# Performance work log

Measured on AMD Instinct MI355X. Metric: run time of the kernel, lower is better.

Reference implementation:

```python
import jax, jax.numpy as jnp
import numpy as np

DIM = 256
N_STATE = 8
DT_RANK = 16  # ceil(dim/16)
D_CONV = 4
HIDDEN = 128  # dim * rank_ratio
EPS = 1e-6


def rmsnorm(x, w):
    # matches torch: x / (||x||_2 / sqrt(d) + eps) * w
    norm = jnp.sqrt(jnp.sum(x * x, axis=-1, keepdims=True))
    return x / (norm / np.sqrt(x.shape[-1]) + EPS) * w


def dwconv1d(x, w, b, pad_l, pad_r):
    # x: (b, l, c); w: (c, 1, k) depthwise
    out = jax.lax.conv_general_dilated(
        x.transpose(0, 2, 1), w, window_strides=(1,),
        padding=[(pad_l, pad_r)], dimension_numbers=('NCH', 'OIH', 'NCH'),
        feature_group_count=w.shape[0])
    return (out + b[None, :, None]).transpose(0, 2, 1)


def selective_scan(x, delta, A, Bm, Cm, D):
    # x, delta: (b,l,d); A: (d,n); Bm, Cm: (b,l,n); D: (d,)
    dA = jnp.exp(delta[..., None] * A)                     # (b,l,d,n)
    dBx = (delta * x)[..., None] * Bm[:, :, None, :]       # (b,l,d,n)

    def step(h, inp):
        dA_t, dBx_t, C_t = inp
        h = dA_t * h + dBx_t                               # (b,d,n)
        y = jnp.einsum('bdn,bn->bd', h, C_t)
        return h, y

    h0 = jnp.zeros((x.shape[0],) + A.shape, dtype=x.dtype)
    _, ys = jax.lax.scan(step, h0,
                         (dA.transpose(1, 0, 2, 3), dBx.transpose(1, 0, 2, 3),
                          Cm.transpose(1, 0, 2)))
    return ys.transpose(1, 0, 2) + x * D                   # (b,l,d)


def mamba_branch(x, ctx, conv_w, conv_b, xproj_w, dtproj_w, dtproj_b, A_log, D):
    xc = jax.nn.silu(dwconv1d(x, conv_w, conv_b, D_CONV - 1, 0))  # causal conv
    x_dbl = ctx @ xproj_w.T                                  # (b,l,r+2n)
    dt, Bm, Cm = jnp.split(x_dbl, [DT_RANK, DT_RANK + N_STATE], axis=-1)
    delta = jax.nn.softplus(dt @ dtproj_w.T + dtproj_b)
    A = -jnp.exp(A_log)
    return selective_scan(xc, delta, A, Bm, Cm, D)


def setup_inputs() -> dict:
    key = jax.random.key(0)
    ks = jax.random.split(key, 24)
    B, L, D = 4, 64 * 64, DIM
    s = 0.02
    A_log_init = jnp.log(jnp.broadcast_to(jnp.arange(1, N_STATE + 1, dtype=jnp.float32), (D, N_STATE)))
    dt_bias = jnp.full((D,), jnp.log(jnp.expm1(0.01)), dtype=jnp.float32)
    inp = {
        'x0': jax.random.normal(ks[0], (B, L, D), jnp.float32),
        'x1': jax.random.normal(ks[1], (B, L, D), jnp.float32),
        'w_norm0': jnp.ones((D,), jnp.float32),
        'w_norm1': jnp.ones((D,), jnp.float32),
        'in_proj_w': jax.random.normal(ks[2], (2 * D, D), jnp.float32) * s,
        'conv_w_f': jax.random.normal(ks[3], (D, 1, D_CONV), jnp.float32) * 0.3,
        'conv_b_f': jnp.zeros((D,), jnp.float32),
        'xproj_w_f': jax.random.normal(ks[4], (DT_RANK + 2 * N_STATE, D), jnp.float32) * s,
        'dtproj_w_f': jax.random.normal(ks[5], (D, DT_RANK), jnp.float32) * 0.1,
        'dtproj_b_f': dt_bias,
        'A_log_f': A_log_init,
        'D_f': jnp.ones((D,), jnp.float32),
        'conv_w_bw': jax.random.normal(ks[6], (D, 1, D_CONV), jnp.float32) * 0.3,
        'conv_b_bw': jnp.zeros((D,), jnp.float32),
        'xproj_w_bw': jax.random.normal(ks[7], (DT_RANK + 2 * N_STATE, D), jnp.float32) * s,
        'dtproj_w_bw': jax.random.normal(ks[8], (D, DT_RANK), jnp.float32) * 0.1,
        'dtproj_b_bw': dt_bias,
        'A_log_bw': A_log_init,
        'D_bw': jnp.ones((D,), jnp.float32),
        'norm_y_w': jnp.ones((D,), jnp.float32),
        'out_proj_w': jax.random.normal(ks[9], (D, D), jnp.float32) * s,
        'fc1_w': jax.random.normal(ks[10], (HIDDEN, D), jnp.float32) * s,
        'dw_w': jax.random.normal(ks[11], (HIDDEN, 1, 3), jnp.float32) * 0.3,
        'dw_b': jnp.zeros((HIDDEN,), jnp.float32),
        'fc2_w': jax.random.normal(ks[12], (D, HIDDEN), jnp.float32) * s,
    }
    return inp


def reference(x0, x1, w_norm0, w_norm1, in_proj_w, conv_w_f, conv_b_f, xproj_w_f,
              dtproj_w_f, dtproj_b_f, A_log_f, D_f, conv_w_bw, conv_b_bw,
              xproj_w_bw, dtproj_w_bw, dtproj_b_bw, A_log_bw, D_bw, norm_y_w,
              out_proj_w, fc1_w, dw_w, dw_b, fc2_w):
    residual = x0
    h0 = rmsnorm(x0, w_norm0)
    h1 = rmsnorm(x1, w_norm1)
    # cross-Mamba: main stream x0 -> x,z; extra_emb x1 -> dt/B/C
    xz = h0 @ in_proj_w.T
    xin, z = jnp.split(xz, 2, axis=-1)
    y_f = mamba_branch(xin, h1, conv_w_f, conv_b_f, xproj_w_f, dtproj_w_f,
                       dtproj_b_f, A_log_f, D_f)
    y_b = jnp.flip(mamba_branch(jnp.flip(xin, 1), jnp.flip(h1, 1), conv_w_bw,
                                conv_b_bw, xproj_w_bw, dtproj_w_bw, dtproj_b_bw,
                                A_log_bw, D_bw), 1)
    y = (y_f + y_b) * 0.5          # if_devide_out=True (bidirectional)
    y = rmsnorm(y, norm_y_w)       # use_norm=True
    y = y * jax.nn.silu(z)
    x = y @ out_proj_w.T + residual
    # LowRankFeedForward (dropout = identity at eval)
    m = x @ fc1_w.T
    m = jax.nn.silu(dwconv1d(m, dw_w, dw_b, 1, 1))
    m = m @ fc2_w.T
    return x + m
```

## Files before the change

### kernel.cpp

```cpp
#include <hip/hip_runtime.h>
#include <math.h>
#include <cstddef>

#define BB 4
#define LL 4096
#define DD 256
#define NST 8
#define RANK 16
#define HID 128
#define BL (BB*LL)
#define BLD ((size_t)BL*DD)
#define CH 256
#define CLEN 16
#define XZS 512

typedef __bf16 bf16x8 __attribute__((ext_vector_type(8)));
typedef float  f32x4  __attribute__((ext_vector_type(4)));

__device__ __forceinline__ float siluf(float x){ return x / (1.f + __expf(-x)); }
__device__ __forceinline__ float softplus_fast(float x){
  float r = __logf(1.f + __expf(x));
  return x > 15.f ? x : r;
}
__device__ __forceinline__ unsigned short f2bf(float x){
  union { float f; unsigned u; } v; v.f = x;
  unsigned r = v.u + 0x7fffu + ((v.u >> 16) & 1u);
  return (unsigned short)(r >> 16);
}
__device__ __forceinline__ float bf2f(unsigned short u){
  union { unsigned u32; float f; } c; c.u32 = ((unsigned)u) << 16;
  return c.f;
}

__global__ __launch_bounds__(256) void pre_kernel(
    const float* __restrict__ x0, const float* __restrict__ w0, unsigned short* __restrict__ o0b,
    const float* __restrict__ x1, const float* __restrict__ w1, unsigned short* __restrict__ o1b,
    const float* __restrict__ sA,
    const float* __restrict__ s0, const float* __restrict__ s1,
    const float* __restrict__ s2, const float* __restrict__ s3,
    const float* __restrict__ s4,
    unsigned short* __restrict__ d1, unsigned short* __restrict__ d2)
{
  int blk = blockIdx.x;
  if (blk < 8192){
    const float* x; const float* w; unsigned short* o; size_t tok;
    int wv = threadIdx.x >> 6, lane = threadIdx.x & 63;
    if (blk < 4096){ x = x0; w = w0; o = o0b; tok = (size_t)blk*4 + wv; }
    else           { x = x1; w = w1; o = o1b; tok = (size_t)(blk-4096)*4 + wv; }
    float4 v = ((const float4*)(x + tok*DD))[lane];
    float s = v.x*v.x + v.y*v.y + v.z*v.z + v.w*v.w;
    #pragma unroll
    for (int m = 1; m < 64; m <<= 1) s += __shfl_xor(s, m, 64);
    float scale = 1.f / (sqrtf(s) * (1.f/16.f) + 1e-6f);
    float4 wvv = ((const float4*)w)[lane];
    ushort4 r;
    r.x = f2bf(v.x*scale*wvv.x); r.y = f2bf(v.y*scale*wvv.y);
    r.z = f2bf(v.z*scale*wvv.z); r.w = f2bf(v.w*scale*wvv.w);
    ((ushort4*)(o + tok*DD))[lane] = r;
    return;
  }
  int i = (blk - 8192)*256 + threadIdx.x;
  if (i >= 278528) return;
  if (i < 131072){ d1[i] = f2bf(sA[i]); return; }
  int j = i - 131072;
  float v;
  if (j < 8192)        v = s0[j];
  else if (j < 16384)  v = s1[j - 8192];
  else if (j < 81920)  v = s2[j - 16384];
  else if (j < 114688) v = s3[j - 81920];
  else                 v = s4[j - 114688];
  d2[j] = f2bf(v);
}

template<int EPI>
__global__ __launch_bounds__(256) void gemm_mfma(
    const unsigned short* __restrict__ A, const unsigned short* __restrict__ Bw,
    float* __restrict__ C, const float* __restrict__ Add,
    unsigned short* __restrict__ Cb, int M, int ldc, int K)
{
  constexpr int BK = 64, PAD = 8;
  __shared__ __align__(16) unsigned short As[64][BK+PAD];
  __shared__ __align__(16) unsigned short Bs[64][BK+PAD];
  int tid  = threadIdx.x;
  int row0 = blockIdx.x * 64;
  int col0 = blockIdx.y * 64;
  int wave = tid >> 6, lane = tid & 63;
  int wm = (wave >> 1) * 32, wn = (wave & 1) * 32;
  int lm = lane & 15, kq = lane >> 4;
  int sr = tid >> 2, sc16 = (tid & 3) * 16;

  f32x4 acc[2][2];
  #pragma unroll
  for (int i = 0; i < 2; i++)
    #pragma unroll
    for (int j = 0; j < 2; j++) acc[i][j] = (f32x4){0.f,0.f,0.f,0.f};

  for (int k0 = 0; k0 < K; k0 += BK){
    const unsigned short* ap = &A [(size_t)(row0 + sr)*K + k0 + sc16];
    const unsigned short* bp = &Bw[(size_t)(col0 + sr)*K + k0 + sc16];
    *(int4*)&As[sr][sc16]   = *(const int4*)ap;
    *(int4*)&As[sr][sc16+8] = *(const int4*)(ap + 8);
    *(int4*)&Bs[sr][sc16]   = *(const int4*)bp;
    *(int4*)&Bs[sr][sc16+8] = *(const int4*)(bp + 8);
    __syncthreads();
    #pragma unroll
    for (int ks = 0; ks < 2; ks++){
      bf16x8 af[2], bfv[2];
      #pragma unroll
      for (int i = 0; i < 2; i++) af[i]  = *(const bf16x8*)&As[wm + i*16 + lm][ks*32 + kq*8];
      #pragma unroll
      for (int j = 0; j < 2; j++) bfv[j] = *(const bf16x8*)&Bs[wn + j*16 + lm][ks*32 + kq*8];
      #pragma unroll
      for (int i = 0; i < 2; i++)
        #pragma unroll
        for (int j = 0; j < 2; j++)
          acc[i][j] = __builtin_amdgcn_mfma_f32_16x16x32_bf16(af[i], bfv[j], acc[i][j], 0, 0, 0);
    }
    __syncthreads();
  }

  #pragma unroll
  for (int i = 0; i < 2; i++){
    int rbase = row0 + wm + i*16 + kq*4;
    #pragma unroll
    for (int j = 0; j < 2; j++){
      int col = col0 + wn + j*16 + lm;
      #pragma unroll
      for (int r = 0; r < 4; r++){
        size_t idx = (size_t)(rbase + r)*ldc + col;
        float v = acc[i][j][r];
        if constexpr (EPI == 2) v += Add[idx];
        if constexpr (EPI != 3) C[idx] = v;
        if constexpr (EPI == 3) Cb[idx] = f2bf(v);
      }
    }
  }
}

__global__ __launch_bounds__(256) void gemm_xzxp(
    const unsigned short* __restrict__ A0, const unsigned short* __restrict__ A1,
    const unsigned short* __restrict__ B0, const unsigned short* __restrict__ B1,
    unsigned short* __restrict__ Cxz, float* __restrict__ Cxd)
{
  constexpr int BK = 64, PAD = 8, K = 256;
  __shared__ __align__(16) unsigned short As[64][BK+PAD];
  __shared__ __align__(16) unsigned short Bs[64][BK+PAD];
  int tid  = threadIdx.x;
  bool xp  = (blockIdx.y == 8);
  const unsigned short* A  = xp ? A1 : A0;
  const unsigned short* Bw = xp ? B1 : B0;
  int row0 = blockIdx.x * 64;
  int col0 = xp ? 0 : blockIdx.y * 64;
  int wave = tid >> 6, lane = tid & 63;
  int wm = (wave >> 1) * 32, wn = (wave & 1) * 32;
  int lm = lane & 15, kq = lane >> 4;
  int sr = tid >> 2, sc16 = (tid & 3) * 16;

  f32x4 acc[2][2];
  #pragma unroll
  for (int i = 0; i < 2; i++)
    #pragma unroll
    for (int j = 0; j < 2; j++) acc[i][j] = (f32x4){0.f,0.f,0.f,0.f};

  for (int k0 = 0; k0 < K; k0 += BK){
    const unsigned short* ap = &A [(size_t)(row0 + sr)*K + k0 + sc16];
    const unsigned short* bp = &Bw[(size_t)(col0 + sr)*K + k0 + sc16];
    *(int4*)&As[sr][sc16]   = *(const int4*)ap;
    *(int4*)&As[sr][sc16+8] = *(const int4*)(ap + 8);
    *(int4*)&Bs[sr][sc16]   = *(const int4*)bp;
    *(int4*)&Bs[sr][sc16+8] = *(const int4*)(bp + 8);
    __syncthreads();
    #pragma unroll
    for (int ks = 0; ks < 2; ks++){
      bf16x8 af[2], bfv[2];
      #pragma unroll
      for (int i = 0; i < 2; i++) af[i]  = *(const bf16x8*)&As[wm + i*16 + lm][ks*32 + kq*8];
      #pragma unroll
      for (int j = 0; j < 2; j++) bfv[j] = *(const bf16x8*)&Bs[wn + j*16 + lm][ks*32 + kq*8];
      #pragma unroll
      for (int i = 0; i < 2; i++)
        #pragma unroll
        for (int j = 0; j < 2; j++)
          acc[i][j] = __builtin_amdgcn_mfma_f32_16x16x32_bf16(af[i], bfv[j], acc[i][j], 0, 0, 0);
    }
    __syncthreads();
  }

  #pragma unroll
  for (int i = 0; i < 2; i++){
    int rbase = row0 + wm + i*16 + kq*4;
    #pragma unroll
    for (int j = 0; j < 2; j++){
      int col = col0 + wn + j*16 + lm;
      #pragma unroll
      for (int r = 0; r < 4; r++){
        float v = acc[i][j][r];
        if (xp) Cxd[(size_t)(rbase + r)*64  + col] = v;
        else    Cxz[(size_t)(rbase + r)*XZS + col] = f2bf(v);
      }
    }
  }
}

__global__ __launch_bounds__(256) void gemm_fc1(
    const float* __restrict__ A, const unsigned short* __restrict__ Bw,
    float* __restrict__ C)
{
  constexpr int BK = 64, PAD = 8, K = 256, LDC = 128;
  __shared__ __align__(16) unsigned short As[64][BK+PAD];
  __shared__ __align__(16) unsigned short Bs[64][BK+PAD];
  int tid  = threadIdx.x;
  int row0 = blockIdx.x * 64;
  int col0 = blockIdx.y * 64;
  int wave = tid >> 6, lane = tid & 63;
  int wm = (wave >> 1) * 32, wn = (wave & 1) * 32;
  int lm = lane & 15, kq = lane >> 4;
  int sr = tid >> 2, sc16 = (tid & 3) * 16;

  f32x4 acc[2][2];
  #pragma unroll
  for (int i = 0; i < 2; i++)
    #pragma unroll
    for (int j = 0; j < 2; j++) acc[i][j] = (f32x4){0.f,0.f,0.f,0.f};

  for (int k0 = 0; k0 < K; k0 += BK){
    const float* ap = &A[(size_t)(row0 + sr)*K + k0 + sc16];
    #pragma unroll
    for (int q = 0; q < 4; q++){
      float4 f = *(const float4*)(ap + q*4);
      ushort4 u; u.x = f2bf(f.x); u.y = f2bf(f.y); u.z = f2bf(f.z); u.w = f2bf(f.w);
      *(ushort4*)&As[sr][sc16 + q*4] = u;
    }
    const unsigned short* bp = &Bw[(size_t)(col0 + sr)*K + k0 + sc16];
    *(int4*)&Bs[sr][sc16]   = *(const int4*)bp;
    *(int4*)&Bs[sr][sc16+8] = *(const int4*)(bp + 8);
    __syncthreads();
    #pragma unroll
    for (int ks = 0; ks < 2; ks++){
      bf16x8 af[2], bfv[2];
      #pragma unroll
      for (int i = 0; i < 2; i++) af[i]  = *(const bf16x8*)&As[wm + i*16 + lm][ks*32 + kq*8];
      #pragma unroll
      for (int j = 0; j < 2; j++) bfv[j] = *(const bf16x8*)&Bs[wn + j*16 + lm][ks*32 + kq*8];
      #pragma unroll
      for (int i = 0; i < 2; i++)
        #pragma unroll
        for (int j = 0; j < 2; j++)
          acc[i][j] = __builtin_amdgcn_mfma_f32_16x16x32_bf16(af[i], bfv[j], acc[i][j], 0, 0, 0);
    }
    __syncthreads();
  }

  #pragma unroll
  for (int i = 0; i < 2; i++){
    int rbase = row0 + wm + i*16 + kq*4;
    #pragma unroll
    for (int j = 0; j < 2; j++){
      int col = col0 + wn + j*16 + lm;
      #pragma unroll
      for (int r = 0; r < 4; r++)
        C[(size_t)(rbase + r)*LDC + col] = acc[i][j][r];
    }
  }
}

__global__ __launch_bounds__(256) void gemm_fc2dw(
    const float* __restrict__ m1, const unsigned short* __restrict__ Bw,
    const float* __restrict__ dww, const float* __restrict__ dwb,
    float* __restrict__ C)
{
  constexpr int BK = 64, PAD = 8, K = 128, LDC = 256;
  __shared__ __align__(16) unsigned short As[64][BK+PAD];
  __shared__ __align__(16) unsigned short Bs[64][BK+PAD];
  __shared__ float wS[HID*3];
  __shared__ float bS[HID];
  int tid  = threadIdx.x;
  if (tid < HID){
    bS[tid] = dwb[tid];
    wS[tid*3+0] = dww[tid*3+0];
    wS[tid*3+1] = dww[tid*3+1];
    wS[tid*3+2] = dww[tid*3+2];
  }
  __syncthreads();

  int row0 = blockIdx.x * 64;
  int col0 = blockIdx.y * 64;
  int wave = tid >> 6, lane = tid & 63;
  int wm = (wave >> 1) * 32, wn = (wave & 1) * 32;
  int lm = lane & 15, kq = lane >> 4;
  int sr = tid >> 2, sc16 = (tid & 3) * 16;
  int r16 = tid >> 4, cc = (tid & 15) * 4;

  f32x4 acc[2][2];
  #pragma unroll
  for (int i = 0; i < 2; i++)
    #pragma unroll
    for (int j = 0; j < 2; j++) acc[i][j] = (f32x4){0.f,0.f,0.f,0.f};

  for (int k0 = 0; k0 < K; k0 += BK){
    #pragma unroll
    for (int pp = 0; pp < 4; pp++){
      int r = pp*16 + r16;
      int t = row0 + r;
      int tl = t & (LL-1);
      int c = k0 + cc;
      const float* mrow = &m1[(size_t)t*HID + c];
      float4 vm = *(const float4*)mrow;
      float4 vp = (tl > 0)      ? *(const float4*)(mrow - HID) : (float4){0,0,0,0};
      float4 vn = (tl < LL-1)   ? *(const float4*)(mrow + HID) : (float4){0,0,0,0};
      float a0 = bS[c+0] + wS[(c+0)*3]*vp.x + wS[(c+0)*3+1]*vm.x + wS[(c+0)*3+2]*vn.x;
      float a1 = bS[c+1] + wS[(c+1)*3]*vp.y + wS[(c+1)*3+1]*vm.y + wS[(c+1)*3+2]*vn.y;
      float a2 = bS[c+2] + wS[(c+2)*3]*vp.z + wS[(c+2)*3+1]*vm.z + wS[(c+2)*3+2]*vn.z;
      float a3 = bS[c+3] + wS[(c+3)*3]*vp.w + wS[(c+3)*3+1]*vm.w + wS[(c+3)*3+2]*vn.w;
      ushort4 u;
      u.x = f2bf(siluf(a0)); u.y = f2bf(siluf(a1));
      u.z = f2bf(siluf(a2)); u.w = f2bf(siluf(a3));
      *(ushort4*)&As[r][cc] = u;
    }
    const unsigned short* bp = &Bw[(size_t)(col0 + sr)*K + k0 + sc16];
    *(int4*)&Bs[sr][sc16]   = *(const int4*)bp;
    *(int4*)&Bs[sr][sc16+8] = *(const int4*)(bp + 8);
    __syncthreads();
    #pragma unroll
    for (int ks = 0; ks < 2; ks++){
      bf16x8 af[2], bfv[2];
      #pragma unroll
      for (int i = 0; i < 2; i++) af[i]  = *(const bf16x8*)&As[wm + i*16 + lm][ks*32 + kq*8];
      #pragma unroll
      for (int j = 0; j < 2; j++) bfv[j] = *(const bf16x8*)&Bs[wn + j*16 + lm][ks*32 + kq*8];
      #pragma unroll
      for (int i = 0; i < 2; i++)
        #pragma unroll
        for (int j = 0; j < 2; j++)
          acc[i][j] = __builtin_amdgcn_mfma_f32_16x16x32_bf16(af[i], bfv[j], acc[i][j], 0, 0, 0);
    }
    __syncthreads();
  }

  #pragma unroll
  for (int i = 0; i < 2; i++){
    int rbase = row0 + wm + i*16 + kq*4;
    #pragma unroll
    for (int j = 0; j < 2; j++){
      int col = col0 + wn + j*16 + lm;
      #pragma unroll
      for (int r = 0; r < 4; r++){
        size_t idx = (size_t)(rbase + r)*LDC + col;
        C[idx] = C[idx] + acc[i][j][r];
      }
    }
  }
}

__global__ __launch_bounds__(256) void front_kernel(
    const unsigned short* __restrict__ xz,
    const float* __restrict__ xd,
    const float* __restrict__ cwf, const float* __restrict__ cbf,
    const float* __restrict__ cwb, const float* __restrict__ cbb,
    const float* __restrict__ dtwf, const float* __restrict__ dtbf,
    const float* __restrict__ dtwb, const float* __restrict__ dtbb,
    const float* __restrict__ Alogf, const float* __restrict__ Alogb,
    const float* __restrict__ Dfp, const float* __restrict__ Dbp,
    unsigned int* __restrict__ xde,
    float* __restrict__ Sp, float* __restrict__ Hout)
{
  int chunk = blockIdx.x, b = blockIdx.y, dir = blockIdx.z;
  int s0 = chunk*CLEN;
  int d  = threadIdx.x;

  __shared__ float sdt[CLEN][16];
  __shared__ float sB [CLEN][8];
  __shared__ float sC [CLEN][8];
  #pragma unroll
  for (int e = threadIdx.x; e < CLEN*32; e += 256){
    int lt = e >> 5, col = e & 31;
    int pos = s0 + lt;
    int row = dir ? (LL-1-pos) : pos;
    float v = xd[((size_t)b*LL + row)*64 + dir*32 + col];
    if (col < 16)      sdt[lt][col]    = v;
    else if (col < 24) sB [lt][col-16] = v;
    else               sC [lt][col-24] = v;
  }
  __syncthreads();

  float4 cw = ((const float4*)(dir ? cwb : cwf))[d];
  float cb  = (dir ? cbb : cbf)[d];
  const float* dtw = (dir ? dtwb : dtwf) + d*RANK;
  float4 w0 = ((const float4*)dtw)[0], w1 = ((const float4*)dtw)[1];
  float4 w2 = ((const float4*)dtw)[2], w3 = ((const float4*)dtw)[3];
  float dtb = (dir ? dtbb : dtbf)[d];
  float Dd  = (dir ? Dbp : Dfp)[d];

  const unsigned short* xp = xz + (size_t)b*LL*XZS + d;
  #define LDX(pos) ((pos) >= 0 ? bf2f(xp[(size_t)(dir ? (LL-1-(pos)) : (pos))*XZS]) : 0.f)

  float xv[CLEN+3];
  xv[0] = LDX(s0-3); xv[1] = LDX(s0-2); xv[2] = LDX(s0-1);
  #pragma unroll
  for (int i = 0; i < CLEN; i++) xv[3+i] = LDX(s0+i);
  #undef LDX

  unsigned packX[CLEN];
  #pragma unroll
  for (int i = 0; i < CLEN; i++){
    float xc = cb;
    xc = fmaf(cw.x, xv[i],   xc); xc = fmaf(cw.y, xv[i+1], xc);
    xc = fmaf(cw.z, xv[i+2], xc); xc = fmaf(cw.w, xv[i+3], xc);
    xc = siluf(xc);
    const float* dt = &sdt[i][0];
    float de = dtb;
    de = fmaf(dt[0],w0.x, fmaf(dt[1],w0.y, fmaf(dt[2],w0.z, fmaf(dt[3],w0.w, de))));
    de = fmaf(dt[4],w1.x, fmaf(dt[5],w1.y, fmaf(dt[6],w1.z, fmaf(dt[7],w1.w, de))));
    de = fmaf(dt[8],w2.x, fmaf(dt[9],w2.y, fmaf(dt[10],w2.z, fmaf(dt[11],w2.w, de))));
    de = fmaf(dt[12],w3.x, fmaf(dt[13],w3.y, fmaf(dt[14],w3.z, fmaf(dt[15],w3.w, de))));
    de = softplus_fast(de);
    packX[i] = (unsigned)f2bf(xc) | ((unsigned)f2bf(de) << 16);
  }

  const float* Alog = dir ? Alogb : Alogf;
  float A[NST];
  bool fast = true;
  #pragma unroll
  for (int n = 0; n < NST; n++){
    A[n] = -__expf(Alog[d*NST + n]);
    fast = fast && (fabsf(A[n] + (float)(n+1)) < 1e-3f);
  }
  float h[NST];
  #pragma unroll
  for (int n = 0; n < NST; n++) h[n] = 0.f;
  float S = 0.f;

  unsigned int* xout = xde + ((size_t)(dir*BB + b)*LL + s0)*DD + d;

  if (fast){
    #pragma unroll
    for (int t = 0; t < CLEN; t++){
      unsigned pk = packX[t];
      float xc = bf2f((unsigned short)(pk & 0xffffu));
      float de = bf2f((unsigned short)(pk >> 16));
      S += de;
      float dux = de * xc;
      const float* Bv = &sB[t][0];
      const float* Cv = &sC[t][0];
      float e1 = __expf(-de);
      float dA = e1;
      float acc = xc * Dd;
      h[0] = fmaf(dA, h[0], dux*Bv[0]); acc = fmaf(h[0], Cv[0], acc); dA *= e1;
      h[1] = fmaf(dA, h[1], dux*Bv[1]); acc = fmaf(h[1], Cv[1], acc); dA *= e1;
      h[2] = fmaf(dA, h[2], dux*Bv[2]); acc = fmaf(h[2], Cv[2], acc); dA *= e1;
      h[3] = fmaf(dA, h[3], dux*Bv[3]); acc = fmaf(h[3], Cv[3], acc); dA *= e1;
      h[4] = fmaf(dA, h[4], dux*Bv[4]); acc = fmaf(h[4], Cv[4], acc); dA *= e1;
      h[5] = fmaf(dA, h[5], dux*Bv[5]); acc = fmaf(h[5], Cv[5], acc); dA *= e1;
      h[6] = fmaf(dA, h[6], dux*Bv[6]); acc = fmaf(h[6], Cv[6], acc); dA *= e1;
      h[7] = fmaf(dA, h[7], dux*Bv[7]); acc = fmaf(h[7], Cv[7], acc);
      xout[(size_t)t*DD] = (pk & 0xffff0000u) | (unsigned)f2bf(acc);
    }
  } else {
    #pragma unroll
    for (int t = 0; t < CLEN; t++){
      unsigned pk = packX[t];
      float xc = bf2f((unsigned short)(pk & 0xffffu));
      float de = bf2f((unsigned short)(pk >> 16));
      S += de;
      float dux = de * xc;
      const float* Bv = &sB[t][0];
      const float* Cv = &sC[t][0];
      float acc = xc * Dd;
      #pragma unroll
      for (int n = 0; n < NST; n++){
        h[n] = fmaf(__expf(de*A[n]), h[n], dux*Bv[n]);
        acc = fmaf(h[n], Cv[n], acc);
      }
      xout[(size_t)t*DD] = (pk & 0xffff0000u) | (unsigned)f2bf(acc);
    }
  }

  size_t ob = ((((size_t)dir*CH + chunk)*BB + b)*DD + d)*NST;
  float4 h0v, h1v;
  h0v.x=h[0]; h0v.y=h[1]; h0v.z=h[2]; h0v.w=h[3];
  h1v.x=h[4]; h1v.y=h[5]; h1v.z=h[6]; h1v.w=h[7];
  *(float4*)&Hout[ob]   = h0v; *(float4*)&Hout[ob+4] = h1v;
  Sp[((size_t)(dir*CH + chunk)*BB + b)*DD + d] = S;
}

__global__ __launch_bounds__(64) void scan_p2(
    const float* __restrict__ Sp, float* H,
    const float* __restrict__ Alogf, const float* __restrict__ Alogb)
{
  const int SEGC = CH/8;
  int blk = blockIdx.x;
  int d   = blk & (DD-1);
  int b   = (blk >> 8) & (BB-1);
  int dir = blk >> 10;
  int t   = threadIdx.x;
  int seg = t >> 3, n = t & 7;
  float A = -__expf((dir ? Alogb : Alogf)[d*NST + n]);

  const size_t sstr = (size_t)BB*DD;
  const size_t hstr = (size_t)BB*DD*NST;
  size_t sb = (size_t)dir*CH*sstr + (size_t)b*DD + d;
  size_t hb = (size_t)dir*CH*hstr + ((size_t)b*DD + d)*NST + n;
  int c0 = seg*SEGC;

  float pv[SEGC], hv[SEGC];
  #pragma unroll
  for (int k = 0; k < SEGC; k++){
    pv[k] = Sp[sb + (size_t)(c0+k)*sstr];
    hv[k] = H [hb + (size_t)(c0+k)*hstr];
  }
  float h = 0.f, Ss = 0.f;
  #pragma unroll
  for (int k = 0; k < SEGC; k++){
    Ss += pv[k];
    pv[k] = __expf(pv[k]*A);
    h = fmaf(pv[k], h, hv[k]);
  }
  float pi = __expf(Ss*A), hi = h;
  #pragma unroll
  for (int off = 8; off < 64; off <<= 1){
    float hprev = __shfl_up(hi, off, 64);
    float pprev = __shfl_up(pi, off, 64);
    if (t >= off){ hi = fmaf(pi, hprev, hi); pi *= pprev; }
  }
  float hin = __shfl_up(hi, 8, 64);
  h = (seg == 0) ? 0.f : hin;
  #pragma unroll
  for (int k = 0; k < SEGC; k++){
    size_t idx = hb + (size_t)(c0+k)*hstr;
    H[idx] = h;
    h = fmaf(pv[k], h, hv[k]);
  }
}

__global__ __launch_bounds__(256) void back_kernel(
    const unsigned int* __restrict__ xde,
    const float* __restrict__ xd,
    const float* __restrict__ Alogf, const float* __restrict__ Alogb,
    const float* __restrict__ Hin,
    const unsigned short* __restrict__ xz,
    const float* __restrict__ wn,
    unsigned short* __restrict__ outb)
{
  int c  = blockIdx.x, b = blockIdx.y;
  int cbk = CH-1-c;
  int d  = threadIdx.x;
  int T0 = c*CLEN;
  int Pb = cbk*CLEN;

  __shared__ float sCf[CLEN][8], sCb[CLEN][8];
  __shared__ float red[CLEN][4];
  __shared__ float sscale[CLEN];
  {
    int k  = threadIdx.x & 7;
    int lt = (threadIdx.x >> 3) & 15;
    if (threadIdx.x < 128)
      sCf[lt][k] = xd[((size_t)b*LL + T0 + lt)*64 + 24 + k];
    else
      sCb[lt][k] = xd[((size_t)b*LL + (T0 + 15 - lt))*64 + 56 + k];
  }
  __syncthreads();

  float Af[NST], Ab[NST];
  bool fast = true;
  #pragma unroll
  for (int n = 0; n < NST; n++){
    Af[n] = -__expf(Alogf[d*NST + n]);
    Ab[n] = -__expf(Alogb[d*NST + n]);
    fast = fast && (fabsf(Af[n] + (float)(n+1)) < 1e-3f)
                && (fabsf(Ab[n] + (float)(n+1)) < 1e-3f);
  }

  float vf[CLEN];

  {
    float hn[NST];
    size_t ib = (((size_t)c*BB + b)*DD + d)*NST;
    float4 a0 = *(const float4*)&Hin[ib];
    float4 a1 = *(const float4*)&Hin[ib+4];
    hn[0]=a0.x; hn[1]=a0.y; hn[2]=a0.z; hn[3]=a0.w;
    hn[4]=a1.x; hn[5]=a1.y; hn[6]=a1.z; hn[7]=a1.w;
    const unsigned int* p = xde + ((size_t)b*LL + T0)*DD + d;
    unsigned int pk[CLEN];
    #pragma unroll
    for (int t = 0; t < CLEN; t++) pk[t] = p[(size_t)t*DD];
    float S = 0.f;
    if (fast){
      #pragma unroll
      for (int t = 0; t < CLEN; t++){
        float y0 = bf2f((unsigned short)(pk[t] & 0xffffu));
        float de = bf2f((unsigned short)(pk[t] >> 16));
        S += de;
        float E = __expf(-S);
        float q = E;
        float corr = q * (hn[0]*sCf[t][0]);
        q *= E; corr = fmaf(q, hn[1]*sCf[t][1], corr);
        q *= E; corr = fmaf(q, hn[2]*sCf[t][2], corr);
        q *= E; corr = fmaf(q, hn[3]*sCf[t][3], corr);
        q *= E; corr = fmaf(q, hn[4]*sCf[t][4], corr);
        q *= E; corr = fmaf(q, hn[5]*sCf[t][5], corr);
        q *= E; corr = fmaf(q, hn[6]*sCf[t][6], corr);
        q *= E; corr = fmaf(q, hn[7]*sCf[t][7], corr);
        vf[t] = y0 + corr;
      }
    } else {
      #pragma unroll
      for (int t = 0; t < CLEN; t++){
        float y0 = bf2f((unsigned short)(pk[t] & 0xffffu));
        float de = bf2f((unsigned short)(pk[t] >> 16));
        S += de;
        float corr = 0.f;
        #pragma unroll
        for (int n = 0; n < NST; n++)
          corr = fmaf(__expf(S*Af[n]), hn[n]*sCf[t][n], corr);
        vf[t] = y0 + corr;
      }
    }
  }

  {
    float hn[NST];
    size_t ib = ((((size_t)CH + cbk)*BB + b)*DD + d)*NST;
    float4 a0 = *(const float4*)&Hin[ib];
    float4 a1 = *(const float4*)&Hin[ib+4];
    hn[0]=a0.x; hn[1]=a0.y; hn[2]=a0.z; hn[3]=a0.w;
    hn[4]=a1.x; hn[5]=a1.y; hn[6]=a1.z; hn[7]=a1.w;
    const unsigned int* p = xde + ((size_t)(BB + b)*LL + Pb)*DD + d;
    unsigned int pk[CLEN];
    #pragma unroll
    for (int t = 0; t < CLEN; t++) pk[t] = p[(size_t)t*DD];
    float S = 0.f;
    if (fast){
      #pragma unroll
      for (int t = 0; t < CLEN; t++){
        float y0 = bf2f((unsigned short)(pk[t] & 0xffffu));
        float de = bf2f((unsigned short)(pk[t] >> 16));
        S += de;
        float E = __expf(-S);
        float q = E;
        float corr = q * (hn[0]*sCb[t][0]);
        q *= E; corr = fmaf(q, hn[1]*sCb[t][1], corr);
        q *= E; corr = fmaf(q, hn[2]*sCb[t][2], corr);
        q *= E; corr = fmaf(q, hn[3]*sCb[t][3], corr);
        q *= E; corr = fmaf(q, hn[4]*sCb[t][4], corr);
        q *= E; corr = fmaf(q, hn[5]*sCb[t][5], corr);
        q *= E; corr = fmaf(q, hn[6]*sCb[t][6], corr);
        q *= E; corr = fmaf(q, hn[7]*sCb[t][7], corr);
        int j = 15 - t;
        vf[j] = 0.5f*(vf[j] + y0 + corr);
      }
    } else {
      #pragma unroll
      for (int t = 0; t < CLEN; t++){
        float y0 = bf2f((unsigned short)(pk[t] & 0xffffu));
        float de = bf2f((unsigned short)(pk[t] >> 16));
        S += de;
        float corr = 0.f;
        #pragma unroll
        for (int n = 0; n < NST; n++)
          corr = fmaf(__expf(S*Ab[n]), hn[n]*sCb[t][n], corr);
        int j = 15 - t;
        vf[j] = 0.5f*(vf[j] + y0 + corr);
      }
    }
  }

  int wave = d >> 6, lane = d & 63;
  #pragma unroll
  for (int j = 0; j < CLEN; j++){
    float s = vf[j]*vf[j];
    #pragma unroll
    for (int m = 1; m < 64; m <<= 1) s += __shfl_xor(s, m, 64);
    if (lane == 0) red[j][wave] = s;
  }
  __syncthreads();
  if (d < CLEN){
    float s = red[d][0] + red[d][1] + red[d][2] + red[d][3];
    sscale[d] = 1.f / (sqrtf(s)*(1.f/16.f) + 1e-6f);
  }
  __syncthreads();

  float wd = wn[d];
  #pragma unroll
  for (int j = 0; j < CLEN; j++){
    size_t tok = (size_t)b*LL + T0 + j;
    float z = bf2f(xz[tok*XZS + 256 + d]);
    outb[tok*DD + d] = f2bf(vf[j]*sscale[j]*wd*siluf(z));
  }
}

extern "C" void kernel_launch(void* const* d_in, const int* in_sizes, int n_in,
                              void* d_out, int out_size, void* d_ws, size_t ws_size,
                              hipStream_t stream)
{
  const float* x0        = (const float*)d_in[0];
  const float* x1        = (const float*)d_in[1];
  const float* w_norm0   = (const float*)d_in[2];
  const float* w_norm1   = (const float*)d_in[3];
  const float* in_proj_w = (const float*)d_in[4];
  const float* conv_w_f  = (const float*)d_in[5];
  const float* conv_b_f  = (const float*)d_in[6];
  const float* xproj_w_f = (const float*)d_in[7];
  const float* dtproj_w_f= (const float*)d_in[8];
  const float* dtproj_b_f= (const float*)d_in[9];
  const float* A_log_f   = (const float*)d_in[10];
  const float* D_f       = (const float*)d_in[11];
  const float* conv_w_bw = (const float*)d_in[12];
  const float* conv_b_bw = (const float*)d_in[13];
  const float* xproj_w_bw= (const float*)d_in[14];
  const float* dtproj_w_bw=(const float*)d_in[15];
  const float* dtproj_b_bw=(const float*)d_in[16];
  const float* A_log_bw  = (const float*)d_in[17];
  const float* D_bw      = (const float*)d_in[18];
  const float* norm_y_w  = (const float*)d_in[19];
  const float* out_proj_w= (const float*)d_in[20];
  const float* fc1_w     = (const float*)d_in[21];
  const float* dw_w      = (const float*)d_in[22];
  const float* dw_b      = (const float*)d_in[23];
  const float* fc2_w     = (const float*)d_in[24];
  float* out = (float*)d_out;
  float* ws  = (float*)d_ws;

  float* r0 = ws + 0*BLD;
  float* r1 = ws + 1*BLD;
  float* r2 = ws + 2*BLD;
  float* r3 = ws + 3*BLD;
  float* r4 = ws + 4*BLD;
  float* r5 = ws + 5*BLD;
  float* r6 = ws + 6*BLD;
  float* r7 = ws + 7*BLD;

  unsigned short* h0b   = (unsigned short*)r0;
  unsigned short* h1b   = (unsigned short*)r1;
  unsigned short* xz_b  = (unsigned short*)r2;
  float*          xd    = r3;
  unsigned int*   xde   = (unsigned int*)r4;
  unsigned short* wbuf1 = (unsigned short*)r6;
  float* Hout = r6;
  float* Hin  = Hout;
  const size_t SPLANE = (size_t)2*CH*BB*DD;
  float* Sp   = r7 + (BLD - SPLANE);
  unsigned short* ycomb_b = (unsigned short*)r0;
  unsigned short* wbuf2   = (unsigned short*)r7;
  unsigned short* wb_xp   = wbuf2;
  unsigned short* wb_out  = wbuf2 + 16384;
  unsigned short* wb_fc1  = wbuf2 + 81920;
  unsigned short* wb_fc2  = wbuf2 + 114688;
  float*          m1      = r4;

  pre_kernel<<<dim3(9280), 256, 0, stream>>>(
      x0, w_norm0, h0b, x1, w_norm1, h1b,
      in_proj_w, xproj_w_f, xproj_w_bw, out_proj_w, fc1_w, fc2_w, wbuf1, wbuf2);

  gemm_xzxp<<<dim3(BL/64, 9), 256, 0, stream>>>(
      h0b, h1b, wbuf1, wb_xp, xz_b, xd);

  front_kernel<<<dim3(CH, BB, 2), 256, 0, stream>>>(
      xz_b, xd, conv_w_f, conv_b_f, conv_w_bw, conv_b_bw,
      dtproj_w_f, dtproj_b_f, dtproj_w_bw, dtproj_b_bw,
      A_log_f, A_log_bw, D_f, D_bw, xde, Sp, Hout);

  scan_p2<<<dim3(2*BB*DD), 64, 0, stream>>>(Sp, Hout, A_log_f, A_log_bw);

  back_kernel<<<dim3(CH, BB), 256, 0, stream>>>(
      xde, xd, A_log_f, A_log_bw, Hin, xz_b, norm_y_w, ycomb_b);

  gemm_mfma<2><<<dim3(BL/64, 4), 256, 0, stream>>>(
      ycomb_b, wb_out, out, x0, nullptr, BL, 256, 256);

  gemm_fc1<<<dim3(BL/64, 2), 256, 0, stream>>>(out, wb_fc1, m1);

  gemm_fc2dw<<<dim3(BL/64, 4), 256, 0, stream>>>(m1, wb_fc2, dw_w, dw_b, out);
}
```

Measured before the change: 251.8 us.

## Load full-K GEMM tiles via global_load_lds into XOR-swizzled LDS

All four GEMM kernels now stage the entire K extent of the A and B tiles into LDS once, replacing the K-loop of 64-wide chunks with one barrier each. Bf16 operands are copied straight from global memory to LDS with the global_load_lds builtin, and the padded layout is replaced by an XOR swizzle to avoid bank conflicts. This removes per-chunk synchronisation and the trip through registers. In exchange LDS use per block rises to about 64KB, which may reduce occupancy, and there is no overlap between loading and MFMA work inside a block.

```diff
diff --git a/kernel.cpp b/kernel.cpp
--- a/kernel.cpp
+++ b/kernel.cpp
@@ -32,6 +32,15 @@
   return c.f;
 }
 
+#define GLD16(gp, lp) __builtin_amdgcn_global_load_lds( \
+    (const __attribute__((address_space(1))) unsigned int*)(gp), \
+    (__attribute__((address_space(3))) unsigned int*)(lp), 16, 0, 0)
+
+#define LDSGK(base, row, g, GPR) \
+  (*(const bf16x8*)((base) + ((((row)*(GPR)) + ((g) ^ ((row)&7))) << 3)))
+#define LDSW4(base, row, col, GPR, u) \
+  *(ushort4*)((base) + ((((row)*(GPR)) + ((((col)>>3)) ^ ((row)&7))) << 3) + ((col)&7)) = (u)
+
 __global__ __launch_bounds__(256) void pre_kernel(
     const float* __restrict__ x0, const float* __restrict__ w0, unsigned short* __restrict__ o0b,
     const float* __restrict__ x1, const float* __restrict__ w1, unsigned short* __restrict__ o1b,
@@ -72,15 +81,140 @@
   d2[j] = f2bf(v);
 }
 
-template<int EPI>
+template<int EPI, int K>
 __global__ __launch_bounds__(256) void gemm_mfma(
     const unsigned short* __restrict__ A, const unsigned short* __restrict__ Bw,
-    float* __restrict__ C, const float* __restrict__ Add,
-    unsigned short* __restrict__ Cb, int M, int ldc, int K)
-{
-  constexpr int BK = 64, PAD = 8;
-  __shared__ __align__(16) unsigned short As[64][BK+PAD];
-  __shared__ __align__(16) unsigned short Bs[64][BK+PAD];
+    float* __restrict__ C, const float* __restrict__ Add, int ldc)
+{
+  constexpr int GPR = K/8;
+  constexpr int NI  = GPR/4;
+  __shared__ __align__(16) unsigned short AsL[64*K];
+  __shared__ __align__(16) unsigned short BsL[64*K];
+  int tid  = threadIdx.x;
+  int row0 = blockIdx.x * 64;
+  int col0 = blockIdx.y * 64;
+  int wave = tid >> 6, lane = tid & 63;
+  int wm = (wave >> 1) * 32, wn = (wave & 1) * 32;
+  int lm = lane & 15, kq = lane >> 4;
+
+  #pragma unroll
+  for (int i = 0; i < NI; i++){
+    int q  = (wave*NI + i)*64 + lane;
+    int r  = q / GPR, gq = q % GPR;
+    int g  = gq ^ (r & 7);
+    GLD16(A  + (size_t)(row0 + r)*K + g*8, AsL + (wave*NI + i)*512);
+    GLD16(Bw + (size_t)(col0 + r)*K + g*8, BsL + (wave*NI + i)*512);
+  }
+  __syncthreads();
+
+  f32x4 acc[2][2];
+  #pragma unroll
+  for (int i = 0; i < 2; i++)
+    #pragma unroll
+    for (int j = 0; j < 2; j++) acc[i][j] = (f32x4){0.f,0.f,0.f,0.f};
+
+  #pragma unroll
+  for (int ks = 0; ks < K/32; ks++){
+    bf16x8 af[2], bfv[2];
+    #pragma unroll
+    for (int i = 0; i < 2; i++) af[i]  = LDSGK(AsL, wm + i*16 + lm, ks*4 + kq, GPR);
+    #pragma unroll
+    for (int j = 0; j < 2; j++) bfv[j] = LDSGK(BsL, wn + j*16 + lm, ks*4 + kq, GPR);
+    #pragma unroll
+    for (int i = 0; i < 2; i++)
+      #pragma unroll
+      for (int j = 0; j < 2; j++)
+        acc[i][j] = __builtin_amdgcn_mfma_f32_16x16x32_bf16(af[i], bfv[j], acc[i][j], 0, 0, 0);
+  }
+
+  #pragma unroll
+  for (int i = 0; i < 2; i++){
+    int rbase = row0 + wm + i*16 + kq*4;
+    #pragma unroll
+    for (int j = 0; j < 2; j++){
+      int col = col0 + wn + j*16 + lm;
+      #pragma unroll
+      for (int r = 0; r < 4; r++){
+        size_t idx = (size_t)(rbase + r)*ldc + col;
+        float v = acc[i][j][r];
+        if constexpr (EPI == 2) v += Add[idx];
+        C[idx] = v;
+      }
+    }
+  }
+}
+
+__global__ __launch_bounds__(256) void gemm_xzxp(
+    const unsigned short* __restrict__ A0i, const unsigned short* __restrict__ A1i,
+    const unsigned short* __restrict__ B0i, const unsigned short* __restrict__ B1i,
+    unsigned short* __restrict__ Cxz, float* __restrict__ Cxd)
+{
+  constexpr int K = 256, GPR = K/8, NI = GPR/4;
+  __shared__ __align__(16) unsigned short AsL[64*K];
+  __shared__ __align__(16) unsigned short BsL[64*K];
+  int tid  = threadIdx.x;
+  bool xp  = (blockIdx.y == 8);
+  const unsigned short* A  = xp ? A1i : A0i;
+  const unsigned short* Bw = xp ? B1i : B0i;
+  int row0 = blockIdx.x * 64;
+  int col0 = xp ? 0 : blockIdx.y * 64;
+  int wave = tid >> 6, lane = tid & 63;
+  int wm = (wave >> 1) * 32, wn = (wave & 1) * 32;
+  int lm = lane & 15, kq = lane >> 4;
+
+  #pragma unroll
+  for (int i = 0; i < NI; i++){
+    int q  = (wave*NI + i)*64 + lane;
+    int r  = q / GPR, gq = q % GPR;
+    int g  = gq ^ (r & 7);
+    GLD16(A  + (size_t)(row0 + r)*K + g*8, AsL + (wave*NI + i)*512);
+    GLD16(Bw + (size_t)(col0 + r)*K + g*8, BsL + (wave*NI + i)*512);
+  }
+  __syncthreads();
+
+  f32x4 acc[2][2];
+  #pragma unroll
+  for (int i = 0; i < 2; i++)
+    #pragma unroll
+    for (int j = 0; j < 2; j++) acc[i][j] = (f32x4){0.f,0.f,0.f,0.f};
+
+  #pragma unroll
+  for (int ks = 0; ks < K/32; ks++){
+    bf16x8 af[2], bfv[2];
+    #pragma unroll
+    for (int i = 0; i < 2; i++) af[i]  = LDSGK(AsL, wm + i*16 + lm, ks*4 + kq, GPR);
+    #pragma unroll
+    for (int j = 0; j < 2; j++) bfv[j] = LDSGK(BsL, wn + j*16 + lm, ks*4 + kq, GPR);
+    #pragma unroll
+    for (int i = 0; i < 2; i++)
+      #pragma unroll
+      for (int j = 0; j < 2; j++)
+        acc[i][j] = __builtin_amdgcn_mfma_f32_16x16x32_bf16(af[i], bfv[j], acc[i][j], 0, 0, 0);
+  }
+
+  #pragma unroll
+  for (int i = 0; i < 2; i++){
+    int rbase = row0 + wm + i*16 + kq*4;
+    #pragma unroll
+    for (int j = 0; j < 2; j++){
+      int col = col0 + wn + j*16 + lm;
+      #pragma unroll
+      for (int r = 0; r < 4; r++){
+        float v = acc[i][j][r];
+        if (xp) Cxd[(size_t)(rbase + r)*64  + col] = v;
+        else    Cxz[(size_t)(rbase + r)*XZS + col] = f2bf(v);
+      }
+    }
+  }
+}
+
+__global__ __launch_bounds__(256) void gemm_fc1(
+    const float* __restrict__ Afp, const unsigned short* __restrict__ Bw,
+    float* __restrict__ C)
+{
+  constexpr int K = 256, GPR = K/8, NI = GPR/4, LDC = 128;
+  __shared__ __align__(16) unsigned short AsL[64*K];
+  __shared__ __align__(16) unsigned short BsL[64*K];
   int tid  = threadIdx.x;
   int row0 = blockIdx.x * 64;
   int col0 = blockIdx.y * 64;
@@ -89,166 +223,43 @@
   int lm = lane & 15, kq = lane >> 4;
   int sr = tid >> 2, sc16 = (tid & 3) * 16;
 
-  f32x4 acc[2][2];
-  #pragma unroll
-  for (int i = 0; i < 2; i++)
-    #pragma unroll
-    for (int j = 0; j < 2; j++) acc[i][j] = (f32x4){0.f,0.f,0.f,0.f};
-
-  for (int k0 = 0; k0 < K; k0 += BK){
-    const unsigned short* ap = &A [(size_t)(row0 + sr)*K + k0 + sc16];
-    const unsigned short* bp = &Bw[(size_t)(col0 + sr)*K + k0 + sc16];
-    *(int4*)&As[sr][sc16]   = *(const int4*)ap;
-    *(int4*)&As[sr][sc16+8] = *(const int4*)(ap + 8);
-    *(int4*)&Bs[sr][sc16]   = *(const int4*)bp;
-    *(int4*)&Bs[sr][sc16+8] = *(const int4*)(bp + 8);
-    __syncthreads();
-    #pragma unroll
-    for (int ks = 0; ks < 2; ks++){
-      bf16x8 af[2], bfv[2];
-      #pragma unroll
-      for (int i = 0; i < 2; i++) af[i]  = *(const bf16x8*)&As[wm + i*16 + lm][ks*32 + kq*8];
-      #pragma unroll
-      for (int j = 0; j < 2; j++) bfv[j] = *(const bf16x8*)&Bs[wn + j*16 + lm][ks*32 + kq*8];
-      #pragma unroll
-      for (int i = 0; i < 2; i++)
-        #pragma unroll
-        for (int j = 0; j < 2; j++)
-          acc[i][j] = __builtin_amdgcn_mfma_f32_16x16x32_bf16(af[i], bfv[j], acc[i][j], 0, 0, 0);
-    }
-    __syncthreads();
-  }
-
-  #pragma unroll
-  for (int i = 0; i < 2; i++){
-    int rbase = row0 + wm + i*16 + kq*4;
-    #pragma unroll
-    for (int j = 0; j < 2; j++){
-      int col = col0 + wn + j*16 + lm;
-      #pragma unroll
-      for (int r = 0; r < 4; r++){
-        size_t idx = (size_t)(rbase + r)*ldc + col;
-        float v = acc[i][j][r];
-        if constexpr (EPI == 2) v += Add[idx];
-        if constexpr (EPI != 3) C[idx] = v;
-        if constexpr (EPI == 3) Cb[idx] = f2bf(v);
-      }
-    }
-  }
-}
-
-__global__ __launch_bounds__(256) void gemm_xzxp(
-    const unsigned short* __restrict__ A0, const unsigned short* __restrict__ A1,
-    const unsigned short* __restrict__ B0, const unsigned short* __restrict__ B1,
-    unsigned short* __restrict__ Cxz, float* __restrict__ Cxd)
-{
-  constexpr int BK = 64, PAD = 8, K = 256;
-  __shared__ __align__(16) unsigned short As[64][BK+PAD];
-  __shared__ __align__(16) unsigned short Bs[64][BK+PAD];
-  int tid  = threadIdx.x;
-  bool xp  = (blockIdx.y == 8);
-  const unsigned short* A  = xp ? A1 : A0;
-  const unsigned short* Bw = xp ? B1 : B0;
-  int row0 = blockIdx.x * 64;
-  int col0 = xp ? 0 : blockIdx.y * 64;
-  int wave = tid >> 6, lane = tid & 63;
-  int wm = (wave >> 1) * 32, wn = (wave & 1) * 32;
-  int lm = lane & 15, kq = lane >> 4;
-  int sr = tid >> 2, sc16 = (tid & 3) * 16;
-
-  f32x4 acc[2][2];
-  #pragma unroll
-  for (int i = 0; i < 2; i++)
-    #pragma unroll
-    for (int j = 0; j < 2; j++) acc[i][j] = (f32x4){0.f,0.f,0.f,0.f};
-
-  for (int k0 = 0; k0 < K; k0 += BK){
-    const unsigned short* ap = &A [(size_t)(row0 + sr)*K + k0 + sc16];
-    const unsigned short* bp = &Bw[(size_t)(col0 + sr)*K + k0 + sc16];
-    *(int4*)&As[sr][sc16]   = *(const int4*)ap;
-    *(int4*)&As[sr][sc16+8] = *(const int4*)(ap + 8);
-    *(int4*)&Bs[sr][sc16]   = *(const int4*)bp;
-    *(int4*)&Bs[sr][sc16+8] = *(const int4*)(bp + 8);
-    __syncthreads();
-    #pragma unroll
-    for (int ks = 0; ks < 2; ks++){
-      bf16x8 af[2], bfv[2];
-      #pragma unroll
-      for (int i = 0; i < 2; i++) af[i]  = *(const bf16x8*)&As[wm + i*16 + lm][ks*32 + kq*8];
-      #pragma unroll
-      for (int j = 0; j < 2; j++) bfv[j] = *(const bf16x8*)&Bs[wn + j*16 + lm][ks*32 + kq*8];
-      #pragma unroll
-      for (int i = 0; i < 2; i++)
-        #pragma unroll
-        for (int j = 0; j < 2; j++)
-          acc[i][j] = __builtin_amdgcn_mfma_f32_16x16x32_bf16(af[i], bfv[j], acc[i][j], 0, 0, 0);
-    }
-    __syncthreads();
-  }
-
-  #pragma unroll
-  for (int i = 0; i < 2; i++){
-    int rbase = row0 + wm + i*16 + kq*4;
-    #pragma unroll
-    for (int j = 0; j < 2; j++){
-      int col = col0 + wn + j*16 + lm;
-      #pragma unroll
-      for (int r = 0; r < 4; r++){
-        float v = acc[i][j][r];
-        if (xp) Cxd[(size_t)(rbase + r)*64  + col] = v;
-        else    Cxz[(size_t)(rbase + r)*XZS + col] = f2bf(v);
-      }
-    }
-  }
-}
-
-__global__ __launch_bounds__(256) void gemm_fc1(
-    const float* __restrict__ A, const unsigned short* __restrict__ Bw,
-    float* __restrict__ C)
-{
-  constexpr int BK = 64, PAD = 8, K = 256, LDC = 128;
-  __shared__ __align__(16) unsigned short As[64][BK+PAD];
-  __shared__ __align__(16) unsigned short Bs[64][BK+PAD];
-  int tid  = threadIdx.x;
-  int row0 = blockIdx.x * 64;
-  int col0 = blockIdx.y * 64;
-  int wave = tid >> 6, lane = tid & 63;
-  int wm = (wave >> 1) * 32, wn = (wave & 1) * 32;
-  int lm = lane & 15, kq = lane >> 4;
-  int sr = tid >> 2, sc16 = (tid & 3) * 16;
-
-  f32x4 acc[2][2];
-  #pragma unroll
-  for (int i = 0; i < 2; i++)
-    #pragma unroll
-    for (int j = 0; j < 2; j++) acc[i][j] = (f32x4){0.f,0.f,0.f,0.f};
-
-  for (int k0 = 0; k0 < K; k0 += BK){
-    const float* ap = &A[(size_t)(row0 + sr)*K + k0 + sc16];
+  #pragma unroll
+  for (int i = 0; i < NI; i++){
+    int q  = (wave*NI + i)*64 + lane;
+    int r  = q / GPR, gq = q % GPR;
+    int g  = gq ^ (r & 7);
+    GLD16(Bw + (size_t)(col0 + r)*K + g*8, BsL + (wave*NI + i)*512);
+  }
+  #pragma unroll
+  for (int k0 = 0; k0 < K; k0 += 64){
+    const float* ap = &Afp[(size_t)(row0 + sr)*K + k0 + sc16];
     #pragma unroll
     for (int q = 0; q < 4; q++){
       float4 f = *(const float4*)(ap + q*4);
       ushort4 u; u.x = f2bf(f.x); u.y = f2bf(f.y); u.z = f2bf(f.z); u.w = f2bf(f.w);
-      *(ushort4*)&As[sr][sc16 + q*4] = u;
-    }
-    const unsigned short* bp = &Bw[(size_t)(col0 + sr)*K + k0 + sc16];
-    *(int4*)&Bs[sr][sc16]   = *(const int4*)bp;
-    *(int4*)&Bs[sr][sc16+8] = *(const int4*)(bp + 8);
-    __syncthreads();
-    #pragma unroll
-    for (int ks = 0; ks < 2; ks++){
-      bf16x8 af[2], bfv[2];
-      #pragma unroll
-      for (int i = 0; i < 2; i++) af[i]  = *(const bf16x8*)&As[wm + i*16 + lm][ks*32 + kq*8];
-      #pragma unroll
-      for (int j = 0; j < 2; j++) bfv[j] = *(const bf16x8*)&Bs[wn + j*16 + lm][ks*32 + kq*8];
-      #pragma unroll
-      for (int i = 0; i < 2; i++)
-        #pragma unroll
-        for (int j = 0; j < 2; j++)
-          acc[i][j] = __builtin_amdgcn_mfma_f32_16x16x32_bf16(af[i], bfv[j], acc[i][j], 0, 0, 0);
-    }
-    __syncthreads();
+      LDSW4(AsL, sr, k0 + sc16 + q*4, GPR, u);
+    }
+  }
+  __syncthreads();
+
+  f32x4 acc[2][2];
+  #pragma unroll
+  for (int i = 0; i < 2; i++)
+    #pragma unroll
+    for (int j = 0; j < 2; j++) acc[i][j] = (f32x4){0.f,0.f,0.f,0.f};
+
+  #pragma unroll
+  for (int ks = 0; ks < K/32; ks++){
+    bf16x8 af[2], bfv[2];
+    #pragma unroll
+    for (int i = 0; i < 2; i++) af[i]  = LDSGK(AsL, wm + i*16 + lm, ks*4 + kq, GPR);
+    #pragma unroll
+    for (int j = 0; j < 2; j++) bfv[j] = LDSGK(BsL, wn + j*16 + lm, ks*4 + kq, GPR);
+    #pragma unroll
+    for (int i = 0; i < 2; i++)
+      #pragma unroll
+      for (int j = 0; j < 2; j++)
+        acc[i][j] = __builtin_amdgcn_mfma_f32_16x16x32_bf16(af[i], bfv[j], acc[i][j], 0, 0, 0);
   }
 
   #pragma unroll
@@ -269,9 +280,9 @@
     const float* __restrict__ dww, const float* __restrict__ dwb,
     float* __restrict__ C)
 {
-  constexpr int BK = 64, PAD = 8, K = 128, LDC = 256;
-  __shared__ __align__(16) unsigned short As[64][BK+PAD];
-  __shared__ __align__(16) unsigned short Bs[64][BK+PAD];
+  constexpr int K = 128, GPR = K/8, NI = GPR/4, LDC = 256;
+  __shared__ __align__(16) unsigned short AsL[64*K];
+  __shared__ __align__(16) unsigned short BsL[64*K];
   __shared__ float wS[HID*3];
   __shared__ float bS[HID];
   int tid  = threadIdx.x;
@@ -281,23 +292,25 @@
     wS[tid*3+1] = dww[tid*3+1];
     wS[tid*3+2] = dww[tid*3+2];
   }
-  __syncthreads();
 
   int row0 = blockIdx.x * 64;
   int col0 = blockIdx.y * 64;
   int wave = tid >> 6, lane = tid & 63;
   int wm = (wave >> 1) * 32, wn = (wave & 1) * 32;
   int lm = lane & 15, kq = lane >> 4;
-  int sr = tid >> 2, sc16 = (tid & 3) * 16;
   int r16 = tid >> 4, cc = (tid & 15) * 4;
 
-  f32x4 acc[2][2];
-  #pragma unroll
-  for (int i = 0; i < 2; i++)
-    #pragma unroll
-    for (int j = 0; j < 2; j++) acc[i][j] = (f32x4){0.f,0.f,0.f,0.f};
-
-  for (int k0 = 0; k0 < K; k0 += BK){
+  #pragma unroll
+  for (int i = 0; i < NI; i++){
+    int q  = (wave*NI + i)*64 + lane;
+    int r  = q / GPR, gq = q % GPR;
+    int g  = gq ^ (r & 7);
+    GLD16(Bw + (size_t)(col0 + r)*K + g*8, BsL + (wave*NI + i)*512);
+  }
+  __syncthreads();
+
+  #pragma unroll
+  for (int k0 = 0; k0 < K; k0 += 64){
     #pragma unroll
     for (int pp = 0; pp < 4; pp++){
       int r = pp*16 + r16;
@@ -315,26 +328,29 @@
       ushort4 u;
       u.x = f2bf(siluf(a0)); u.y = f2bf(siluf(a1));
       u.z = f2bf(siluf(a2)); u.w = f2bf(siluf(a3));
-      *(ushort4*)&As[r][cc] = u;
-    }
-    const unsigned short* bp = &Bw[(size_t)(col0 + sr)*K + k0 + sc16];
-    *(int4*)&Bs[sr][sc16]   = *(const int4*)bp;
-    *(int4*)&Bs[sr][sc16+8] = *(const int4*)(bp + 8);
-    __syncthreads();
-    #pragma unroll
-    for (int ks = 0; ks < 2; ks++){
-      bf16x8 af[2], bfv[2];
-      #pragma unroll
-      for (int i = 0; i < 2; i++) af[i]  = *(const bf16x8*)&As[wm + i*16 + lm][ks*32 + kq*8];
-      #pragma unroll
-      for (int j = 0; j < 2; j++) bfv[j] = *(const bf16x8*)&Bs[wn + j*16 + lm][ks*32 + kq*8];
-      #pragma unroll
-      for (int i = 0; i < 2; i++)
-        #pragma unroll
-        for (int j = 0; j < 2; j++)
-          acc[i][j] = __builtin_amdgcn_mfma_f32_16x16x32_bf16(af[i], bfv[j], acc[i][j], 0, 0, 0);
-    }
-    __syncthreads();
+      LDSW4(AsL, r, c, GPR, u);
+    }
+  }
+  __syncthreads();
+
+  f32x4 acc[2][2];
+  #pragma unroll
+  for (int i = 0; i < 2; i++)
+    #pragma unroll
+    for (int j = 0; j < 2; j++) acc[i][j] = (f32x4){0.f,0.f,0.f,0.f};
+
+  #pragma unroll
+  for (int ks = 0; ks < K/32; ks++){
+    bf16x8 af[2], bfv[2];
+    #pragma unroll
+    for (int i = 0; i < 2; i++) af[i]  = LDSGK(AsL, wm + i*16 + lm, ks*4 + kq, GPR);
+    #pragma unroll
+    for (int j = 0; j < 2; j++) bfv[j] = LDSGK(BsL, wn + j*16 + lm, ks*4 + kq, GPR);
+    #pragma unroll
+    for (int i = 0; i < 2; i++)
+      #pragma unroll
+      for (int j = 0; j < 2; j++)
+        acc[i][j] = __builtin_amdgcn_mfma_f32_16x16x32_bf16(af[i], bfv[j], acc[i][j], 0, 0, 0);
   }
 
   #pragma unroll
@@ -764,8 +780,8 @@
   back_kernel<<<dim3(CH, BB), 256, 0, stream>>>(
       xde, xd, A_log_f, A_log_bw, Hin, xz_b, norm_y_w, ycomb_b);
 
-  gemm_mfma<2><<<dim3(BL/64, 4), 256, 0, stream>>>(
-      ycomb_b, wb_out, out, x0, nullptr, BL, 256, 256);
+  gemm_mfma<2, 256><<<dim3(BL/64, 4), 256, 0, stream>>>(
+      ycomb_b, wb_out, out, x0, 256);
 
   gemm_fc1<<<dim3(BL/64, 2), 256, 0, stream>>>(out, wb_fc1, m1);
 
```

Result: no change. 251.1 us (-0.3%).
